# Kernel optimization log

Measured on AMD Instinct MI355X. Metric: run time of the kernel, lower is better.

The kernel has to match this reference:

```python
import jax, jax.numpy as jnp
import numpy as np

B, L, D, H, MLP = 8, 1024, 768, 12, 3072
DH = D // H
EPS = 1e-5


def setup_inputs() -> dict:
    key = jax.random.key(0)
    ks = jax.random.split(key, 8)
    s = 0.02
    return {
        "x": jax.random.normal(ks[0], (B, L, D), dtype=jnp.float32),
        "ln1_g": jnp.ones((D,), jnp.float32),
        "ln1_b": jnp.zeros((D,), jnp.float32),
        "w_qkv": jax.random.normal(ks[1], (3 * D, D), dtype=jnp.float32) * s,
        "w_out": jax.random.normal(ks[2], (D, D), dtype=jnp.float32) * s,
        "b_out": jnp.zeros((D,), jnp.float32),
        "ln2_g": jnp.ones((D,), jnp.float32),
        "ln2_b": jnp.zeros((D,), jnp.float32),
        "w1": jax.random.normal(ks[3], (MLP, D), dtype=jnp.float32) * s,
        "b1": jnp.zeros((MLP,), jnp.float32),
        "w2": jax.random.normal(ks[4], (D, MLP), dtype=jnp.float32) * s,
        "b2": jnp.zeros((D,), jnp.float32),
    }


def _layernorm(x, g, b):
    mu = jnp.mean(x, axis=-1, keepdims=True)
    var = jnp.mean(jnp.square(x - mu), axis=-1, keepdims=True)
    return (x - mu) * jax.lax.rsqrt(var + EPS) * g + b


def reference(x, ln1_g, ln1_b, w_qkv, w_out, b_out, ln2_g, ln2_b, w1, b1, w2, b2):
    # --- self-attention branch ---
    xn = _layernorm(x, ln1_g, ln1_b)                     # [B, L, D]
    qkv = jnp.einsum('bld,ed->ble', xn, w_qkv)           # [B, L, 3D]
    # rearrange 'b l (qkv h d) -> qkv b h l d'
    qkv = qkv.reshape(B, L, 3, H, DH).transpose(2, 0, 3, 1, 4)
    q, k, v = qkv[0], qkv[1], qkv[2]                     # [B, H, L, DH]
    scale = DH ** -0.5
    att = jnp.einsum('bhxd,bhyd->bhxy', q, k) * scale    # [B, H, L, L]
    att = jax.nn.softmax(att, axis=-1)
    o = jnp.einsum('bhxy,bhyd->bhxd', att, v)            # [B, H, L, DH]
    o = o.transpose(0, 2, 1, 3).reshape(B, L, D)         # 'b h l d -> b l (h d)'
    o = jnp.einsum('bld,ed->ble', o, w_out) + b_out
    x = x + o
    # --- MLP branch ---
    xn = _layernorm(x, ln2_g, ln2_b)
    h = jax.nn.gelu(jnp.einsum('bld,md->blm', xn, w1) + b1, approximate=False)
    h = jnp.einsum('blm,dm->bld', h, w2) + b2
    return x + h
```

## Files before the change

kernel.cpp:

```cpp
#include <hip/hip_runtime.h>
#include <hip/hip_bf16.h>
#include <math.h>

#define NB 8
#define NL 1024
#define ND 768
#define NH 12
#define NDH 64
#define NMLP 3072
#define NROWS 8192

typedef __attribute__((ext_vector_type(8))) short short8;
typedef __attribute__((ext_vector_type(8))) __bf16 bf16x8;
typedef __attribute__((ext_vector_type(4))) float f32x4;
typedef __attribute__((ext_vector_type(4))) float float4v;
typedef __attribute__((ext_vector_type(4))) unsigned short ushort4v;

__device__ __forceinline__ unsigned short f2b(float f) {
  unsigned u = __float_as_uint(f);
  unsigned r = (u + 0x7fffu + ((u >> 16) & 1u)) >> 16;
  return (unsigned short)r;
}

__device__ __forceinline__ f32x4 mfma16(short8 a, short8 b, f32x4 c) {
  return __builtin_amdgcn_mfma_f32_16x16x32_bf16(
      __builtin_bit_cast(bf16x8, a), __builtin_bit_cast(bf16x8, b), c, 0, 0, 0);
}

__device__ __forceinline__ void gl_lds16(const void* g, void* l) {
  __builtin_amdgcn_global_load_lds(
      (__attribute__((address_space(1))) void*)g,
      (__attribute__((address_space(3))) void*)l, 16, 0, 0);
}

__global__ __launch_bounds__(256) void cvt_all(const float* __restrict__ s0,
                                               const float* __restrict__ s1,
                                               const float* __restrict__ s2,
                                               const float* __restrict__ s3,
                                               unsigned short* __restrict__ d) {
  int i = (blockIdx.x * 256 + threadIdx.x) * 4;
  const float* s;
  int off;
  if (i < 1769472) { s = s0; off = i; }
  else if (i < 2359296) { s = s1; off = i - 1769472; }
  else if (i < 4718592) { s = s2; off = i - 2359296; }
  else { s = s3; off = i - 4718592; }
  float4v v = *(const float4v*)(s + off);
  ushort4v o;
  o[0] = f2b(v[0]); o[1] = f2b(v[1]); o[2] = f2b(v[2]); o[3] = f2b(v[3]);
  *(ushort4v*)(d + i) = o;
}

__global__ __launch_bounds__(256) void ln_bf16(const float* __restrict__ x,
                                               const float* __restrict__ g,
                                               const float* __restrict__ b,
                                               unsigned short* __restrict__ out) {
  int row = blockIdx.x, tid = threadIdx.x;
  const float* xr = x + (size_t)row * ND;
  float v0 = xr[tid], v1 = xr[tid + 256], v2 = xr[tid + 512];
  float s = v0 + v1 + v2;
  __shared__ float red[8];
#pragma unroll
  for (int o = 32; o > 0; o >>= 1) s += __shfl_down(s, o);
  int wv = tid >> 6, ln = tid & 63;
  if (ln == 0) red[wv] = s;
  __syncthreads();
  float mu = (red[0] + red[1] + red[2] + red[3]) * (1.0f / 768.0f);
  float d0 = v0 - mu, d1 = v1 - mu, d2 = v2 - mu;
  float q = d0 * d0 + d1 * d1 + d2 * d2;
#pragma unroll
  for (int o = 32; o > 0; o >>= 1) q += __shfl_down(q, o);
  if (ln == 0) red[4 + wv] = q;
  __syncthreads();
  float var = (red[4] + red[5] + red[6] + red[7]) * (1.0f / 768.0f);
  float rs = rsqrtf(var + 1e-5f);
  unsigned short* orow = out + (size_t)row * ND;
  orow[tid]       = f2b(d0 * rs * g[tid]       + b[tid]);
  orow[tid + 256] = f2b(d1 * rs * g[tid + 256] + b[tid + 256]);
  orow[tid + 512] = f2b(d2 * rs * g[tid + 512] + b[tid + 512]);
}

template <int MODE>
__global__ __launch_bounds__(256) void gemm_bt(
    const unsigned short* __restrict__ A, const unsigned short* __restrict__ W,
    unsigned short* __restrict__ outB, const float* __restrict__ bias,
    int M, int N, int K, int gx) {
  __shared__ __attribute__((aligned(16))) unsigned short As[3 * 4096];
  __shared__ __attribute__((aligned(16))) unsigned short Bs[3 * 4096];

  const int nwg = gridDim.x;
  const int bid = blockIdx.x;
  const int q = nwg >> 3, r = nwg & 7;
  const int xcd = bid & 7, idx = bid >> 3;
  const int swz = (xcd < r ? xcd * (q + 1) : r * (q + 1) + (xcd - r) * q) + idx;
  const int by = swz / gx, bx = swz - by * gx;
  const int m0 = by * 128, n0 = bx * 128;

  const int tid = threadIdx.x;
  const int wave = tid >> 6, lane = tid & 63;
  const int l15 = lane & 15, lhi = lane >> 4;
  const int wm = wave >> 1, wn = wave & 1;

  const int sr = tid >> 2, sc8 = (tid & 3) * 8;
  const unsigned short* Ag0 = A + (size_t)(m0 + sr) * K + sc8;
  const unsigned short* Ag1 = Ag0 + (size_t)64 * K;
  const unsigned short* Wg0 = W + (size_t)(n0 + sr) * K + sc8;
  const unsigned short* Wg1 = Wg0 + (size_t)64 * K;

  f32x4 acc[4][4];
#pragma unroll
  for (int i = 0; i < 4; i++)
#pragma unroll
    for (int j = 0; j < 4; j++) acc[i][j] = (f32x4){0.f, 0.f, 0.f, 0.f};

  auto STAGE = [&](int kelem, int buf) {
    unsigned short* Ad = As + buf * 4096 + wave * 512;
    unsigned short* Bd = Bs + buf * 4096 + wave * 512;
    gl_lds16(Ag0 + kelem, Ad);
    gl_lds16(Ag1 + kelem, Ad + 2048);
    gl_lds16(Wg0 + kelem, Bd);
    gl_lds16(Wg1 + kelem, Bd + 2048);
  };

  const int NT = K >> 5;
  STAGE(0, 0);
  STAGE(32, 1);

  int cb = 0, nbuf = 2;
  for (int t = 0; t < NT; ++t) {
    if (t + 2 < NT) {
      STAGE((t + 2) * 32, nbuf);
      asm volatile("s_waitcnt vmcnt(8)" ::: "memory");
    } else if (t + 2 == NT) {
      asm volatile("s_waitcnt vmcnt(4)" ::: "memory");
    } else {
      asm volatile("s_waitcnt vmcnt(0)" ::: "memory");
    }
    __builtin_amdgcn_s_barrier();

    const unsigned short* Ac = As + cb * 4096;
    const unsigned short* Bc = Bs + cb * 4096;
    short8 af[4], bf[4];
#pragma unroll
    for (int i = 0; i < 4; i++)
      af[i] = *(const short8*)&Ac[(wm * 64 + i * 16 + l15) * 32 + lhi * 8];
#pragma unroll
    for (int j = 0; j < 4; j++)
      bf[j] = *(const short8*)&Bc[(wn * 64 + j * 16 + l15) * 32 + lhi * 8];
#pragma unroll
    for (int i = 0; i < 4; i++)
#pragma unroll
      for (int j = 0; j < 4; j++) acc[i][j] = mfma16(af[i], bf[j], acc[i][j]);

    asm volatile("s_waitcnt lgkmcnt(0)" ::: "memory");
    __builtin_amdgcn_s_barrier();
    cb = (cb == 2) ? 0 : cb + 1;
    nbuf = (nbuf == 2) ? 0 : nbuf + 1;
  }

#pragma unroll
  for (int i = 0; i < 4; i++) {
    int row = m0 + wm * 64 + i * 16 + lhi * 4;
#pragma unroll
    for (int j = 0; j < 4; j++) {
      int col = n0 + wn * 64 + j * 16 + l15;
#pragma unroll
      for (int r2 = 0; r2 < 4; r2++) {
        float v = acc[i][j][r2];
        size_t idxo = (size_t)(row + r2) * N + col;
        if (MODE == 0) {
          outB[idxo] = f2b(v);
        } else {
          float t2 = v + bias[col];
          float z = 1.5957691f * t2 * (1.0f + 0.044715f * t2 * t2);
          float e = __expf(-z);
          outB[idxo] = f2b(__fdividef(t2, 1.0f + e));
        }
      }
    }
  }
}

template <int MODE>
__global__ __launch_bounds__(256) void gemm_bt64(
    const unsigned short* __restrict__ A, const unsigned short* __restrict__ W,
    float* __restrict__ outF, const float* __restrict__ bias,
    const float* __restrict__ resid, int M, int N, int K, int gx) {
  __shared__ __attribute__((aligned(16))) unsigned short As[2 * 4096];
  __shared__ __attribute__((aligned(16))) unsigned short Bs[2 * 8192];

  const int nwg = gridDim.x;
  const int bid = blockIdx.x;
  const int q = nwg >> 3, r = nwg & 7;
  const int xcd = bid & 7, idx = bid >> 3;
  const int swz = (xcd < r ? xcd * (q + 1) : r * (q + 1) + (xcd - r) * q) + idx;
  const int by = swz / gx, bx = swz - by * gx;
  const int m0 = by * 64, n0 = bx * 128;

  const int tid = threadIdx.x;
  const int wave = tid >> 6, lane = tid & 63;
  const int l15 = lane & 15, lhi = lane >> 4;
  const int wn = wave;

  const int sr = tid >> 3;
  const int swc8 = ((tid & 7) ^ (sr & 7)) * 8;
  const unsigned short* Aga = A + (size_t)(m0 + sr) * K + swc8;
  const unsigned short* Wga = W + (size_t)(n0 + sr) * K + swc8;

  f32x4 acc[4][2];
#pragma unroll
  for (int i = 0; i < 4; i++)
#pragma unroll
    for (int j = 0; j < 2; j++) acc[i][j] = (f32x4){0.f, 0.f, 0.f, 0.f};

  auto STAGE = [&](int kelem, int buf) {
    unsigned short* Ad = As + buf * 4096 + wave * 512;
    unsigned short* Bd = Bs + buf * 8192 + wave * 512;
    gl_lds16(Aga + kelem, Ad);
    gl_lds16(Aga + (size_t)32 * K + kelem, Ad + 2048);
    gl_lds16(Wga + kelem, Bd);
    gl_lds16(Wga + (size_t)32 * K + kelem, Bd + 2048);
    gl_lds16(Wga + (size_t)64 * K + kelem, Bd + 4096);
    gl_lds16(Wga + (size_t)96 * K + kelem, Bd + 6144);
  };

  const int NT = K >> 6;
  STAGE(0, 0);

  for (int t = 0; t < NT; ++t) {
    const int cb = t & 1;
    if (t + 1 < NT) {
      STAGE((t + 1) * 64, cb ^ 1);
      asm volatile("s_waitcnt vmcnt(6)" ::: "memory");
    } else {
      asm volatile("s_waitcnt vmcnt(0)" ::: "memory");
    }
    __builtin_amdgcn_s_barrier();

    const unsigned short* Ac = As + cb * 4096;
    const unsigned short* Bc = Bs + cb * 8192;
    short8 af[4][2], bf[2][2];
#pragma unroll
    for (int i = 0; i < 4; i++) {
      int ar = i * 16 + l15;
#pragma unroll
      for (int kk = 0; kk < 2; kk++)
        af[i][kk] = *(const short8*)&Ac[ar * 64 + (((kk * 4 + lhi) ^ (ar & 7)) * 8)];
    }
#pragma unroll
    for (int j = 0; j < 2; j++) {
      int br = wn * 32 + j * 16 + l15;
#pragma unroll
      for (int kk = 0; kk < 2; kk++)
        bf[j][kk] = *(const short8*)&Bc[br * 64 + (((kk * 4 + lhi) ^ (br & 7)) * 8)];
    }
#pragma unroll
    for (int kk = 0; kk < 2; kk++)
#pragma unroll
      for (int i = 0; i < 4; i++)
#pragma unroll
        for (int j = 0; j < 2; j++)
          acc[i][j] = mfma16(af[i][kk], bf[j][kk], acc[i][j]);

    asm volatile("s_waitcnt lgkmcnt(0)" ::: "memory");
    __builtin_amdgcn_s_barrier();
  }

#pragma unroll
  for (int i = 0; i < 4; i++) {
    int row = m0 + i * 16 + lhi * 4;
#pragma unroll
    for (int j = 0; j < 2; j++) {
      int col = n0 + wn * 32 + j * 16 + l15;
#pragma unroll
      for (int r2 = 0; r2 < 4; r2++) {
        size_t idxo = (size_t)(row + r2) * N + col;
        outF[idxo] = acc[i][j][r2] + bias[col] + resid[idxo];
      }
    }
  }
}

__global__ __launch_bounds__(256) void vtrans(const unsigned short* __restrict__ qkv,
                                              unsigned short* __restrict__ vT) {
  int bid = blockIdx.x;
  int tt = bid & 15;
  int t2 = bid >> 4;
  int h = t2 % NH, b = t2 / NH;
  __shared__ unsigned short L[64 * 72];
  int t = threadIdx.x;
  int row0 = t >> 3;
  int col8 = (t & 7) * 8;
#pragma unroll
  for (int s = 0; s < 2; s++) {
    int row = row0 + s * 32;
    const unsigned short* src =
        qkv + ((size_t)(b * NL + tt * 64 + row)) * 2304 + 1536 + h * 64 + col8;
    short8 v = *(const short8*)src;
    int wchunk = row >> 3;
#pragma unroll
    for (int j = 0; j < 8; j++) {
      int d = col8 + j;
      int cp = wchunk ^ (d >> 3);
      L[d * 72 + cp * 8 + (row & 7)] = (unsigned short)v[j];
    }
  }
  __syncthreads();
#pragma unroll
  for (int s = 0; s < 2; s++) {
    int d = (t >> 3) + s * 32;
    int rc = t & 7;
    int cp = rc ^ (d >> 3);
    short8 ov = *(const short8*)&L[d * 72 + cp * 8];
    *(short8*)(vT + ((size_t)((b * NH + h) * 64 + d)) * NL + tt * 64 + rc * 8) = ov;
  }
}

__global__ __launch_bounds__(256, 3) void attn_kernel(
    const unsigned short* __restrict__ qkv, const unsigned short* __restrict__ vT,
    unsigned short* __restrict__ o) {
  int bid = blockIdx.x;
  int qt = bid & 7;
  int t = bid >> 3;
  int h = t % NH, b = t / NH;
  const int tid = threadIdx.x;
  const int wave = tid >> 6, lane = tid & 63;
  const int l15 = lane & 15, lhi = lane >> 4;
  const int sw = l15 & 7;
  __shared__ __attribute__((aligned(16))) unsigned short Ks[2 * 64 * 64];
  __shared__ __attribute__((aligned(16))) unsigned short Vs[2 * 64 * 64];
  __shared__ __attribute__((aligned(16))) unsigned short Ps[4 * 16 * 64];

  const unsigned short* qp = qkv + (size_t)(b * NL + qt * 128) * 2304 + h * 64;
  short8 qf[2][2];
#pragma unroll
  for (int i = 0; i < 2; i++)
#pragma unroll
    for (int kk = 0; kk < 2; kk++)
      qf[i][kk] = *(const short8*)(qp + (size_t)(i * 64 + wave * 16 + l15) * 2304 +
                                   kk * 32 + lhi * 8);

  const int srow = tid >> 3, scpos = tid & 7;
  const int sc8 = (scpos ^ (srow & 7)) * 8;
  const unsigned short* ks0 =
      qkv + (size_t)(b * NL + srow) * 2304 + 768 + h * 64 + sc8;
  const unsigned short* vt0 =
      vT + (size_t)((b * NH + h) * 64 + srow) * NL + sc8;
  unsigned short* Pw = Ps + wave * 1024;

  float mrow[2][4];
  f32x4 acc[2][4];
  f32x4 accL[2];
#pragma unroll
  for (int i = 0; i < 2; i++) {
#pragma unroll
    for (int r = 0; r < 4; r++) mrow[i][r] = -1e30f;
    accL[i] = (f32x4){0.f, 0.f, 0.f, 0.f};
#pragma unroll
    for (int nb = 0; nb < 4; nb++) acc[i][nb] = (f32x4){0.f, 0.f, 0.f, 0.f};
  }

  short8 onesf;
#pragma unroll
  for (int j = 0; j < 8; j++) onesf[j] = (short)0x3F80;

#define STAGE(ktile, buf)                                                    \
  {                                                                          \
    const unsigned short* ksrc = ks0 + (size_t)((ktile) * 64) * 2304;        \
    const unsigned short* vsrc = vt0 + (ktile) * 64;                         \
    unsigned short* kb_ = Ks + (buf) * 4096 + wave * 512;                    \
    unsigned short* vb_ = Vs + (buf) * 4096 + wave * 512;                    \
    gl_lds16(ksrc, kb_);                                                     \
    gl_lds16(ksrc + (size_t)32 * 2304, kb_ + 2048);                          \
    gl_lds16(vsrc, vb_);                                                     \
    gl_lds16(vsrc + 32 * NL, vb_ + 2048);                                    \
  }

  STAGE(0, 0);

  for (int kt = 0; kt < 16; kt++) {
    const int cb = kt & 1;
    if (kt + 1 < 16) {
      STAGE(kt + 1, cb ^ 1);
      asm volatile("s_waitcnt vmcnt(4)" ::: "memory");
    } else {
      asm volatile("s_waitcnt vmcnt(0)" ::: "memory");
    }
    __builtin_amdgcn_s_barrier();

    const unsigned short* Kc = Ks + cb * 4096;
    const unsigned short* Vc = Vs + cb * 4096;

    short8 vf[4][2];
#pragma unroll
    for (int nb = 0; nb < 4; nb++)
#pragma unroll
      for (int kk = 0; kk < 2; kk++)
        vf[nb][kk] =
            *(const short8*)&Vc[(nb * 16 + l15) * 64 + ((kk * 4 + lhi) ^ sw) * 8];

#pragma unroll
    for (int i = 0; i < 2; i++) {
      f32x4 sv[4];
#pragma unroll
      for (int kb = 0; kb < 4; kb++) {
        short8 kf0 = *(const short8*)&Kc[(kb * 16 + l15) * 64 + (lhi ^ sw) * 8];
        short8 kf1 = *(const short8*)&Kc[(kb * 16 + l15) * 64 + ((4 + lhi) ^ sw) * 8];
        f32x4 s = mfma16(qf[i][0], kf0, (f32x4){0.f, 0.f, 0.f, 0.f});
        sv[kb] = mfma16(qf[i][1], kf1, s);
      }
      float xmax[4];
#pragma unroll
      for (int r = 0; r < 4; r++) {
        float x = fmaxf(fmaxf(sv[0][r], sv[1][r]), fmaxf(sv[2][r], sv[3][r]));
#pragma unroll
        for (int m = 1; m < 16; m <<= 1) x = fmaxf(x, __shfl_xor(x, m));
        xmax[r] = x;
      }
      bool ok = (xmax[0] <= mrow[i][0] + 64.f) & (xmax[1] <= mrow[i][1] + 64.f) &
                (xmax[2] <= mrow[i][2] + 64.f) & (xmax[3] <= mrow[i][3] + 64.f);
      if (!__all(ok)) {
#pragma unroll
        for (int r = 0; r < 4; r++) {
          float mnew = fmaxf(mrow[i][r], xmax[r]);
          float corr = __expf((mrow[i][r] - mnew) * 0.125f);
          mrow[i][r] = mnew;
#pragma unroll
          for (int nb = 0; nb < 4; nb++) acc[i][nb][r] *= corr;
          accL[i][r] *= corr;
        }
      }
      float mm[4];
#pragma unroll
      for (int r = 0; r < 4; r++) mm[r] = -mrow[i][r] * 0.125f;
#pragma unroll
      for (int kb = 0; kb < 4; kb++) {
        int ch = kb * 2 + (l15 >> 3);
#pragma unroll
        for (int r = 0; r < 4; r++) {
          int row = lhi * 4 + r;
          float p = __expf(fmaf(sv[kb][r], 0.125f, mm[r]));
          unsigned short pu =
              (unsigned short)((__float_as_uint(p) + 0x8000u) >> 16);
          Pw[row * 64 + ((ch ^ (row & 7)) << 3) + sw] = pu;
        }
      }
      short8 pf0 = *(const short8*)&Pw[l15 * 64 + (lhi ^ sw) * 8];
      short8 pf1 = *(const short8*)&Pw[l15 * 64 + ((4 + lhi) ^ sw) * 8];
#pragma unroll
      for (int nb = 0; nb < 4; nb++) {
        acc[i][nb] = mfma16(pf0, vf[nb][0], acc[i][nb]);
        acc[i][nb] = mfma16(pf1, vf[nb][1], acc[i][nb]);
      }
      accL[i] = mfma16(pf0, onesf, accL[i]);
      accL[i] = mfma16(pf1, onesf, accL[i]);
    }
    __builtin_amdgcn_s_barrier();
  }
#undef STAGE

#pragma unroll
  for (int i = 0; i < 2; i++) {
    float inv[4];
#pragma unroll
    for (int r = 0; r < 4; r++) inv[r] = 1.0f / accL[i][r];
    size_t obase =
        (size_t)(b * NL + qt * 128 + i * 64 + wave * 16 + lhi * 4) * ND + h * 64;
#pragma unroll
    for (int nb = 0; nb < 4; nb++)
#pragma unroll
      for (int r = 0; r < 4; r++)
        o[obase + (size_t)r * ND + nb * 16 + l15] = f2b(acc[i][nb][r] * inv[r]);
  }
}

extern "C" void kernel_launch(void* const* d_in, const int* in_sizes, int n_in,
                              void* d_out, int out_size, void* d_ws, size_t ws_size,
                              hipStream_t stream) {
  const float* x     = (const float*)d_in[0];
  const float* ln1_g = (const float*)d_in[1];
  const float* ln1_b = (const float*)d_in[2];
  const float* w_qkv = (const float*)d_in[3];
  const float* w_out = (const float*)d_in[4];
  const float* b_out = (const float*)d_in[5];
  const float* ln2_g = (const float*)d_in[6];
  const float* ln2_b = (const float*)d_in[7];
  const float* w1    = (const float*)d_in[8];
  const float* b1    = (const float*)d_in[9];
  const float* w2    = (const float*)d_in[10];
  const float* b2    = (const float*)d_in[11];
  float* out = (float*)d_out;

  char* p = (char*)d_ws;
  unsigned short* wqkv_b = (unsigned short*)p; p += (size_t)2304 * 768 * 2;
  unsigned short* wout_b = (unsigned short*)p; p += (size_t)768 * 768 * 2;
  unsigned short* w1_b   = (unsigned short*)p; p += (size_t)3072 * 768 * 2;
  unsigned short* w2_b   = (unsigned short*)p; p += (size_t)768 * 3072 * 2;
  unsigned short* xn     = (unsigned short*)p; p += (size_t)NROWS * ND * 2;
  unsigned short* qkvb   = (unsigned short*)p; p += (size_t)NROWS * NMLP * 2;
  float* x1 = (float*)p;  p += (size_t)NROWS * ND * 4;
  unsigned short* vTb = (unsigned short*)x1;

  cvt_all<<<7077888 / 4 / 256, 256, 0, stream>>>(w_qkv, w_out, w1, w2, wqkv_b);

  ln_bf16<<<NROWS, 256, 0, stream>>>(x, ln1_g, ln1_b, xn);
  gemm_bt<0><<<1152, 256, 0, stream>>>(
      xn, wqkv_b, qkvb, nullptr, NROWS, 2304, 768, 18);
  vtrans<<<NB * NH * (NL / 64), 256, 0, stream>>>(qkvb, vTb);
  attn_kernel<<<NB * NH * (NL / 128), 256, 0, stream>>>(qkvb, vTb, xn);
  gemm_bt64<1><<<768, 256, 0, stream>>>(
      xn, wout_b, x1, b_out, x, NROWS, 768, 768, 6);
  ln_bf16<<<NROWS, 256, 0, stream>>>(x1, ln2_g, ln2_b, xn);
  gemm_bt<2><<<1536, 256, 0, stream>>>(
      xn, w1_b, qkvb, b1, NROWS, 3072, 768, 24);
  gemm_bt64<3><<<768, 256, 0, stream>>>(
      qkvb, w2_b, out, b2, x1, NROWS, 768, 3072, 6);
}
```

Before: 273.1 us.

## Restructure attention loop into QK, softmax, PV phases with priority hints

Result: no change. 273.0 us (-0.0%).

```diff
diff --git a/kernel.cpp b/kernel.cpp
--- a/kernel.cpp
+++ b/kernel.cpp
@@ -316,12 +316,14 @@
   }
 }
 
+#define L2E8 0.180336880f
 __global__ __launch_bounds__(256, 3) void attn_kernel(
     const unsigned short* __restrict__ qkv, const unsigned short* __restrict__ vT,
     unsigned short* __restrict__ o) {
-  int bid = blockIdx.x;
-  int qt = bid & 7;
-  int t = bid >> 3;
+  int bid0 = blockIdx.x;
+  int lb = (bid0 & 7) * 96 + (bid0 >> 3);
+  int qt = lb & 7;
+  int t = lb >> 3;
   int h = t % NH, b = t / NH;
   const int tid = threadIdx.x;
   const int wave = tid >> 6, lane = tid & 63;
@@ -329,7 +331,7 @@
   const int sw = l15 & 7;
   __shared__ __attribute__((aligned(16))) unsigned short Ks[2 * 64 * 64];
   __shared__ __attribute__((aligned(16))) unsigned short Vs[2 * 64 * 64];
-  __shared__ __attribute__((aligned(16))) unsigned short Ps[4 * 16 * 64];
+  __shared__ __attribute__((aligned(16))) unsigned short Ps[2 * 4 * 16 * 64];
 
   const unsigned short* qp = qkv + (size_t)(b * NL + qt * 128) * 2304 + h * 64;
   short8 qf[2][2];
@@ -346,7 +348,8 @@
       qkv + (size_t)(b * NL + srow) * 2304 + 768 + h * 64 + sc8;
   const unsigned short* vt0 =
       vT + (size_t)((b * NH + h) * 64 + srow) * NL + sc8;
-  unsigned short* Pw = Ps + wave * 1024;
+  unsigned short* Pw0 = Ps + wave * 1024;
+  unsigned short* Pw1 = Ps + 4096 + wave * 1024;
 
   float mrow[2][4];
   f32x4 acc[2][4];
@@ -391,6 +394,20 @@
     const unsigned short* Kc = Ks + cb * 4096;
     const unsigned short* Vc = Vs + cb * 4096;
 
+    f32x4 sv[2][4];
+    __builtin_amdgcn_s_setprio(1);
+#pragma unroll
+    for (int kb = 0; kb < 4; kb++) {
+      short8 kf0 = *(const short8*)&Kc[(kb * 16 + l15) * 64 + (lhi ^ sw) * 8];
+      short8 kf1 = *(const short8*)&Kc[(kb * 16 + l15) * 64 + ((4 + lhi) ^ sw) * 8];
+#pragma unroll
+      for (int i = 0; i < 2; i++) {
+        f32x4 s = mfma16(qf[i][0], kf0, (f32x4){0.f, 0.f, 0.f, 0.f});
+        sv[i][kb] = mfma16(qf[i][1], kf1, s);
+      }
+    }
+    __builtin_amdgcn_s_setprio(0);
+
     short8 vf[4][2];
 #pragma unroll
     for (int nb = 0; nb < 4; nb++)
@@ -401,18 +418,12 @@
 
 #pragma unroll
     for (int i = 0; i < 2; i++) {
-      f32x4 sv[4];
-#pragma unroll
-      for (int kb = 0; kb < 4; kb++) {
-        short8 kf0 = *(const short8*)&Kc[(kb * 16 + l15) * 64 + (lhi ^ sw) * 8];
-        short8 kf1 = *(const short8*)&Kc[(kb * 16 + l15) * 64 + ((4 + lhi) ^ sw) * 8];
-        f32x4 s = mfma16(qf[i][0], kf0, (f32x4){0.f, 0.f, 0.f, 0.f});
-        sv[kb] = mfma16(qf[i][1], kf1, s);
-      }
+      unsigned short* Pw = i ? Pw1 : Pw0;
       float xmax[4];
 #pragma unroll
       for (int r = 0; r < 4; r++) {
-        float x = fmaxf(fmaxf(sv[0][r], sv[1][r]), fmaxf(sv[2][r], sv[3][r]));
+        float x = fmaxf(fmaxf(sv[i][0][r], sv[i][1][r]),
+                        fmaxf(sv[i][2][r], sv[i][3][r]));
 #pragma unroll
         for (int m = 1; m < 16; m <<= 1) x = fmaxf(x, __shfl_xor(x, m));
         xmax[r] = x;
@@ -423,7 +434,7 @@
 #pragma unroll
         for (int r = 0; r < 4; r++) {
           float mnew = fmaxf(mrow[i][r], xmax[r]);
-          float corr = __expf((mrow[i][r] - mnew) * 0.125f);
+          float corr = exp2f((mrow[i][r] - mnew) * L2E8);
           mrow[i][r] = mnew;
 #pragma unroll
           for (int nb = 0; nb < 4; nb++) acc[i][nb][r] *= corr;
@@ -432,19 +443,25 @@
       }
       float mm[4];
 #pragma unroll
-      for (int r = 0; r < 4; r++) mm[r] = -mrow[i][r] * 0.125f;
+      for (int r = 0; r < 4; r++) mm[r] = -mrow[i][r] * L2E8;
 #pragma unroll
       for (int kb = 0; kb < 4; kb++) {
         int ch = kb * 2 + (l15 >> 3);
 #pragma unroll
         for (int r = 0; r < 4; r++) {
           int row = lhi * 4 + r;
-          float p = __expf(fmaf(sv[kb][r], 0.125f, mm[r]));
+          float p = exp2f(fmaf(sv[i][kb][r], L2E8, mm[r]));
           unsigned short pu =
               (unsigned short)((__float_as_uint(p) + 0x8000u) >> 16);
           Pw[row * 64 + ((ch ^ (row & 7)) << 3) + sw] = pu;
         }
       }
+    }
+
+    __builtin_amdgcn_s_setprio(1);
+#pragma unroll
+    for (int i = 0; i < 2; i++) {
+      const unsigned short* Pw = i ? Pw1 : Pw0;
       short8 pf0 = *(const short8*)&Pw[l15 * 64 + (lhi ^ sw) * 8];
       short8 pf1 = *(const short8*)&Pw[l15 * 64 + ((4 + lhi) ^ sw) * 8];
 #pragma unroll
@@ -455,6 +472,7 @@
       accL[i] = mfma16(pf0, onesf, accL[i]);
       accL[i] = mfma16(pf1, onesf, accL[i]);
     }
+    __builtin_amdgcn_s_setprio(0);
     __builtin_amdgcn_s_barrier();
   }
 #undef STAGE
```
